# Kernel tuning notes

Hardware: AMD Instinct MI355X
Metric: run time of the kernel (lower is better)

## Reference

```python
import jax, jax.numpy as jnp
import numpy as np

N_NODES = 100000
N_EDGES = 600000
IN_FEAT = 128
OUT_FEAT = 128
NUM_RELS = 8
NUM_BASES = 4


def setup_inputs() -> dict:
    key = jax.random.key(0)
    ks = jax.random.split(key, 8)
    h = jax.random.normal(ks[0], (N_NODES, IN_FEAT), dtype=jnp.float32)
    # xavier-ish scale for params
    weight = jax.random.normal(ks[1], (NUM_BASES, IN_FEAT, OUT_FEAT), dtype=jnp.float32) * (1.0 / np.sqrt(IN_FEAT))
    w_comp = jax.random.normal(ks[2], (NUM_RELS, NUM_BASES), dtype=jnp.float32) * (1.0 / np.sqrt(NUM_BASES))
    root_weight = jax.random.normal(ks[3], (IN_FEAT, OUT_FEAT), dtype=jnp.float32) * (1.0 / np.sqrt(IN_FEAT))
    bias = jnp.zeros((OUT_FEAT,), dtype=jnp.float32)
    src = jax.random.randint(ks[4], (N_EDGES,), 0, N_NODES, dtype=jnp.int32)
    dst = jax.random.randint(ks[5], (N_EDGES,), 0, N_NODES, dtype=jnp.int32)
    rel_type = jax.random.randint(ks[6], (N_EDGES,), 0, NUM_RELS, dtype=jnp.int32)
    return {"h": h, "weight": weight, "w_comp": w_comp, "root_weight": root_weight,
            "bias": bias, "src": src, "dst": dst, "rel_type": rel_type}


def reference(h, weight, w_comp, root_weight, bias, src, dst, rel_type):
    # Basis decomposition: W[r] = sum_b w_comp[r,b] * weight[b]
    B, I, O = weight.shape
    R = w_comp.shape[0]
    W = (w_comp @ weight.reshape(B, I * O)).reshape(R, I, O)  # [R, in, out]
    # msg_e = h[src_e] @ W[rel_e]; computed as all-relation projection + gather
    # (avoids materializing [E, in, out] per-edge weights)
    proj = jnp.einsum('ni,rio->nro', h, W)          # [N, R, out]
    msg = proj[src, rel_type]                        # [E, out]
    agg = jax.ops.segment_sum(msg, dst, num_segments=h.shape[0])  # scatter-sum
    out = h @ root_weight + agg + bias
    return jax.nn.relu(out)
```

## Files before the change

### kernel.cpp

```cpp
#include <hip/hip_runtime.h>
#include <hip/hip_bf16.h>

#define N_NODES 100000
#define N_EDGES 600000
#define FEAT 128
#define NUM_RELS 8
#define NUM_BASES 4
#define NBE 2344

#define PREP_CAST 6250
#define PREP_BLDB 320
#define PREP_ZERO 392
#define PREP_GRID (PREP_CAST + PREP_BLDB + PREP_ZERO)

#define SCAN_TILES 98

typedef short bf16x8 __attribute__((ext_vector_type(8)));
typedef float f32x4  __attribute__((ext_vector_type(4)));
typedef float f32x2  __attribute__((ext_vector_type(2)));

__device__ inline short f2bf(float x) {
    __hip_bfloat16 b = __float2bfloat16(x);
    return *reinterpret_cast<short*>(&b);
}


__global__ __launch_bounds__(256) void k_prep(const float* __restrict__ h,
                                              const float* __restrict__ weight,
                                              const float* __restrict__ rw,
                                              short* __restrict__ hb,
                                              short* __restrict__ Bt,
                                              int* __restrict__ cnt,
                                              int* __restrict__ status) {
    int b = blockIdx.x;
    if (b < PREP_CAST) {
        int i = b * 256 + threadIdx.x;
        const float4* h4 = (const float4*)h;
        float4 v0 = h4[2 * i], v1 = h4[2 * i + 1];
        union { short s[8]; bf16x8 v; } u;
        u.s[0] = f2bf(v0.x); u.s[1] = f2bf(v0.y); u.s[2] = f2bf(v0.z); u.s[3] = f2bf(v0.w);
        u.s[4] = f2bf(v1.x); u.s[5] = f2bf(v1.y); u.s[6] = f2bf(v1.z); u.s[7] = f2bf(v1.w);
        ((bf16x8*)hb)[i] = u.v;
    } else if (b < PREP_CAST + PREP_BLDB) {
        int idx = (b - PREP_CAST) * 256 + threadIdx.x;
        int kc = idx >> 14;
        int e  = idx & 16383;
        int o  = e >> 7, ip = e & 127;
        float v = (kc == 0) ? rw[ip * FEAT + o]
                            : weight[(kc - 1) * FEAT * FEAT + ip * FEAT + o];
        Bt[idx] = f2bf(v);
    } else {
        int i = (b - PREP_CAST - PREP_BLDB) * 256 + threadIdx.x;
        if (i < N_NODES) cnt[i] = 0;
        else if (i - N_NODES < 128) status[i - N_NODES] = 0;
    }
}

__global__ __launch_bounds__(256) void k_hist_dst(const int* __restrict__ dst,
                                                  int* __restrict__ cnt) {
    int i = blockIdx.x * 256 + threadIdx.x;
    if (i < N_EDGES) atomicAdd(&cnt[dst[i]], 1);
}

__global__ __launch_bounds__(256) void k_scan_lb(const int* __restrict__ cnt,
                                                 int* __restrict__ offs,
                                                 int* __restrict__ cursor,
                                                 int* __restrict__ status) {
    __shared__ int wsum[4];
    __shared__ int bcast;
    int bid = blockIdx.x;
    int lane = threadIdx.x & 63, wid = threadIdx.x >> 6;
    const int N4 = N_NODES / 4;
    int i4 = bid * 256 + threadIdx.x;

    const int4* cnt4 = (const int4*)cnt;
    int4 v = (i4 < N4) ? cnt4[i4] : make_int4(0, 0, 0, 0);
    int s = v.x + v.y + v.z + v.w;
    int incl = s;
#pragma unroll
    for (int d = 1; d < 64; d <<= 1) {
        int t = __shfl_up(incl, d);
        if (lane >= d) incl += t;
    }
    if (lane == 63) wsum[wid] = incl;
    __syncthreads();
    if (threadIdx.x == 0) {
        int a = 0;
#pragma unroll
        for (int w = 0; w < 4; ++w) { int x = wsum[w]; wsum[w] = a; a += x; }
        int total = a;
        __hip_atomic_store(&status[bid], (total << 2) | 1,
                           __ATOMIC_RELEASE, __HIP_MEMORY_SCOPE_AGENT);
        int excl = 0;
        for (int t = bid - 1; t >= 0; ) {
            int st = __hip_atomic_load(&status[t],
                                       __ATOMIC_ACQUIRE, __HIP_MEMORY_SCOPE_AGENT);
            if ((st & 3) == 0) { __builtin_amdgcn_s_sleep(1); continue; }
            excl += st >> 2;
            if ((st & 3) == 2) break;
            --t;
        }
        __hip_atomic_store(&status[bid], ((excl + total) << 2) | 2,
                           __ATOMIC_RELEASE, __HIP_MEMORY_SCOPE_AGENT);
        bcast = excl;
        if (bid == SCAN_TILES - 1) offs[N_NODES] = excl + total;
    }
    __syncthreads();
    int base = bcast + wsum[wid] + incl - s;
    if (i4 < N4) {
        int4 ex;
        ex.x = base;
        ex.y = base + v.x;
        ex.z = base + v.x + v.y;
        ex.w = base + v.x + v.y + v.z;
        ((int4*)offs)[i4]   = ex;
        ((int4*)cursor)[i4] = ex;
    }
}

__global__ __launch_bounds__(256) void k_scatter_sorted(const int* __restrict__ src,
                                                        const int* __restrict__ dst,
                                                        const int* __restrict__ rel,
                                                        int* __restrict__ cursor,
                                                        int* __restrict__ packed) {
    int e = blockIdx.x * 256 + threadIdx.x;
    if (e < N_EDGES) {
        int p = atomicAdd(&cursor[dst[e]], 1);
        packed[p] = (src[e] << 3) | rel[e];
    }
}

__global__ __launch_bounds__(256) void k_edge_z(const int* __restrict__ offs,
                                                const int* __restrict__ packed,
                                                const float* __restrict__ wc,
                                                const short* __restrict__ hb,
                                                unsigned int* __restrict__ z_u32) {
    int wid = threadIdx.x >> 6, lane = threadIdx.x & 63;
    int d = blockIdx.x * 4 + wid;
    if (d >= N_NODES) return;
    int s = offs[d], e = offs[d + 1];

    const float4* wc4 = (const float4*)wc;
    const unsigned int* hbu = (const unsigned int*)hb;

    f32x2 z2[4] = {(f32x2)0.f, (f32x2)0.f, (f32x2)0.f, (f32x2)0.f};

    for (int base = s; base < e; base += 64) {
        int rem = e - base;
        int m = rem < 64 ? rem : 64;
        int pk = (lane < m) ? packed[base + lane] : 0;
        int j = 0;
        for (; j + 3 < m; j += 4) {
            int p0 = __builtin_amdgcn_readlane(pk, j);
            int p1 = __builtin_amdgcn_readlane(pk, j + 1);
            int p2 = __builtin_amdgcn_readlane(pk, j + 2);
            int p3 = __builtin_amdgcn_readlane(pk, j + 3);
            unsigned int v0 = hbu[(size_t)(p0 >> 3) * 64 + lane];
            unsigned int v1 = hbu[(size_t)(p1 >> 3) * 64 + lane];
            unsigned int v2 = hbu[(size_t)(p2 >> 3) * 64 + lane];
            unsigned int v3 = hbu[(size_t)(p3 >> 3) * 64 + lane];
            float4 c0 = wc4[p0 & 7];
            float4 c1 = wc4[p1 & 7];
            float4 c2 = wc4[p2 & 7];
            float4 c3 = wc4[p3 & 7];
            f32x2 h0; h0.x = __int_as_float(v0 << 16); h0.y = __int_as_float(v0 & 0xffff0000u);
            f32x2 h1; h1.x = __int_as_float(v1 << 16); h1.y = __int_as_float(v1 & 0xffff0000u);
            f32x2 h2; h2.x = __int_as_float(v2 << 16); h2.y = __int_as_float(v2 & 0xffff0000u);
            f32x2 h3; h3.x = __int_as_float(v3 << 16); h3.y = __int_as_float(v3 & 0xffff0000u);
            f32x2 cc;
            cc = c0.x; z2[0] += cc * h0;
            cc = c0.y; z2[1] += cc * h0;
            cc = c0.z; z2[2] += cc * h0;
            cc = c0.w; z2[3] += cc * h0;
            cc = c1.x; z2[0] += cc * h1;
            cc = c1.y; z2[1] += cc * h1;
            cc = c1.z; z2[2] += cc * h1;
            cc = c1.w; z2[3] += cc * h1;
            cc = c2.x; z2[0] += cc * h2;
            cc = c2.y; z2[1] += cc * h2;
            cc = c2.z; z2[2] += cc * h2;
            cc = c2.w; z2[3] += cc * h2;
            cc = c3.x; z2[0] += cc * h3;
            cc = c3.y; z2[1] += cc * h3;
            cc = c3.z; z2[2] += cc * h3;
            cc = c3.w; z2[3] += cc * h3;
        }
        for (; j < m; ++j) {
            int p0 = __builtin_amdgcn_readlane(pk, j);
            unsigned int v0 = hbu[(size_t)(p0 >> 3) * 64 + lane];
            float4 c0 = wc4[p0 & 7];
            f32x2 h0; h0.x = __int_as_float(v0 << 16); h0.y = __int_as_float(v0 & 0xffff0000u);
            f32x2 cc;
            cc = c0.x; z2[0] += cc * h0;
            cc = c0.y; z2[1] += cc * h0;
            cc = c0.z; z2[2] += cc * h0;
            cc = c0.w; z2[3] += cc * h0;
        }
    }

    unsigned int* row = z_u32 + (size_t)d * 256;
#pragma unroll
    for (int b = 0; b < 4; ++b) {
        unsigned int lo = ((unsigned int)(unsigned short)f2bf(z2[b].x));
        unsigned int hi = ((unsigned int)(unsigned short)f2bf(z2[b].y)) << 16;
        row[b * 64 + lane] = lo | hi;
    }
}

__global__ __launch_bounds__(256) void k_gemm_fused(const short* __restrict__ hb,
                                                    const short* __restrict__ z,
                                                    const short* __restrict__ Bt,
                                                    const float* __restrict__ bias,
                                                    float* __restrict__ out) {
    __shared__ short lds[FEAT * FEAT];
    int wave = threadIdx.x >> 6, lane = threadIdx.x & 63;
    int quad = lane >> 4, n16 = lane & 15;
    int base = blockIdx.x * 128 + wave * 32;

    int rowA0 = base + n16;        if (rowA0 >= N_NODES) rowA0 = N_NODES - 1;
    int rowA1 = base + 16 + n16;   if (rowA1 >= N_NODES) rowA1 = N_NODES - 1;

    f32x4 acc[2][8];
#pragma unroll
    for (int mt = 0; mt < 2; ++mt)
#pragma unroll
        for (int nt = 0; nt < 8; ++nt) acc[mt][nt] = (f32x4)0.f;

    float4* l4 = (float4*)lds;
    const bf16x8* bp = (const bf16x8*)lds;

    for (int kc = 0; kc < 5; ++kc) {
        if (kc) __syncthreads();
        const float4* s4 = (const float4*)(Bt + kc * FEAT * FEAT);
#pragma unroll
        for (int t = 0; t < 8; ++t) {
            int linear = threadIdx.x + t * 256;
            int o = linear >> 4, c = linear & 15;
            l4[(o << 4) + ((c + (o >> 3)) & 15)] = s4[linear];
        }
        __syncthreads();

        const bf16x8* a0p = (kc == 0)
            ? (const bf16x8*)(hb + (size_t)rowA0 * FEAT)
            : (const bf16x8*)(z + (size_t)rowA0 * 512 + (kc - 1) * FEAT);
        const bf16x8* a1p = (kc == 0)
            ? (const bf16x8*)(hb + (size_t)rowA1 * FEAT)
            : (const bf16x8*)(z + (size_t)rowA1 * 512 + (kc - 1) * FEAT);

#pragma unroll
        for (int ks = 0; ks < 4; ++ks) {
            bf16x8 a0 = a0p[ks * 4 + quad];
            bf16x8 a1 = a1p[ks * 4 + quad];
            int sw = (ks * 4 + quad + n16) & 15;
#pragma unroll
            for (int nt = 0; nt < 8; ++nt) {
                int o = n16 * 8 + nt;
                bf16x8 b = bp[(o << 4) + sw];
                acc[0][nt] = __builtin_amdgcn_mfma_f32_16x16x32_bf16(a0, b, acc[0][nt], 0, 0, 0);
                acc[1][nt] = __builtin_amdgcn_mfma_f32_16x16x32_bf16(a1, b, acc[1][nt], 0, 0, 0);
            }
        }
    }

    float bv[8];
#pragma unroll
    for (int nt = 0; nt < 8; ++nt) bv[nt] = bias[n16 * 8 + nt];

#pragma unroll
    for (int mt = 0; mt < 2; ++mt)
#pragma unroll
        for (int reg = 0; reg < 4; ++reg) {
            int node = base + mt * 16 + quad * 4 + reg;
            if (node < N_NODES) {
                float4 fa, fb;
                fa.x = fmaxf(acc[mt][0][reg] + bv[0], 0.f);
                fa.y = fmaxf(acc[mt][1][reg] + bv[1], 0.f);
                fa.z = fmaxf(acc[mt][2][reg] + bv[2], 0.f);
                fa.w = fmaxf(acc[mt][3][reg] + bv[3], 0.f);
                fb.x = fmaxf(acc[mt][4][reg] + bv[4], 0.f);
                fb.y = fmaxf(acc[mt][5][reg] + bv[5], 0.f);
                fb.z = fmaxf(acc[mt][6][reg] + bv[6], 0.f);
                fb.w = fmaxf(acc[mt][7][reg] + bv[7], 0.f);
                float* row = out + (size_t)node * FEAT + n16 * 8;
                *(float4*)row       = fa;
                *(float4*)(row + 4) = fb;
            }
        }
}


extern "C" void kernel_launch(void* const* d_in, const int* in_sizes, int n_in,
                              void* d_out, int out_size, void* d_ws, size_t ws_size,
                              hipStream_t stream) {
    const float* h    = (const float*)d_in[0];
    const float* wgt  = (const float*)d_in[1];
    const float* wcmp = (const float*)d_in[2];
    const float* rw   = (const float*)d_in[3];
    const float* bias = (const float*)d_in[4];
    const int*   src  = (const int*)d_in[5];
    const int*   dst  = (const int*)d_in[6];
    const int*   rel  = (const int*)d_in[7];
    float* out = (float*)d_out;

    char* ws = (char*)d_ws;
    short*        hb     = (short*)(ws + 0);
    short*        Bt     = (short*)(ws + 25600000ull);
    short*        z      = (short*)(ws + 25763840ull);
    unsigned int* z_u32  = (unsigned int*)z;
    int*          packed = (int*)(ws + 128163840ull);
    int*          cnt    = (int*)(ws + 130563840ull);
    int*          offs   = (int*)(ws + 130963840ull);
    int*          cursor = (int*)(ws + 131363968ull);
    int*          status = (int*)(ws + 131763968ull);

    hipLaunchKernelGGL(k_prep,     dim3(PREP_GRID), dim3(256), 0, stream,
                       h, wgt, rw, hb, Bt, cnt, status);
    hipLaunchKernelGGL(k_hist_dst, dim3(NBE),  dim3(256), 0, stream, dst, cnt);
    hipLaunchKernelGGL(k_scan_lb,  dim3(SCAN_TILES), dim3(256), 0, stream,
                       cnt, offs, cursor, status);
    hipLaunchKernelGGL(k_scatter_sorted, dim3(NBE), dim3(256), 0, stream,
                       src, dst, rel, cursor, packed);
    hipLaunchKernelGGL(k_edge_z,   dim3((N_NODES + 3) / 4), dim3(256), 0, stream,
                       offs, packed, wcmp, hb, z_u32);
    hipLaunchKernelGGL(k_gemm_fused, dim3((N_NODES + 127) / 128), dim3(256), 0, stream,
                       hb, z, Bt, bias, out);
}
```

Baseline: 270.7 us.

## Pre-swizzle B in global memory and stage it with direct global-to-LDS loads

The prep kernel now writes the bf16 weight matrix already in the swizzled LDS layout. The GEMM then copies it with global_load_lds DMA instead of a register round trip. Each block's tile drops from 128 to 64 rows, so the grid doubles and each wave uses fewer accumulator registers, which may raise occupancy. The cost is that every block now reloads all five 32KB B chunks for half as many rows, roughly doubling B traffic and barrier count per unit of work.

```diff
diff --git a/kernel.cpp b/kernel.cpp
--- a/kernel.cpp
+++ b/kernel.cpp
@@ -48,7 +48,9 @@
         int o  = e >> 7, ip = e & 127;
         float v = (kc == 0) ? rw[ip * FEAT + o]
                             : weight[(kc - 1) * FEAT * FEAT + ip * FEAT + o];
-        Bt[idx] = f2bf(v);
+        int c = ip >> 3, r = ip & 7;
+        int L = (o << 4) | ((c + (o >> 3)) & 15);
+        Bt[kc * 16384 + L * 8 + r] = f2bf(v);
     } else {
         int i = (b - PREP_CAST - PREP_BLDB) * 256 + threadIdx.x;
         if (i < N_NODES) cnt[i] = 0;
@@ -215,49 +217,44 @@
     __shared__ short lds[FEAT * FEAT];
     int wave = threadIdx.x >> 6, lane = threadIdx.x & 63;
     int quad = lane >> 4, n16 = lane & 15;
-    int base = blockIdx.x * 128 + wave * 32;
-
-    int rowA0 = base + n16;        if (rowA0 >= N_NODES) rowA0 = N_NODES - 1;
-    int rowA1 = base + 16 + n16;   if (rowA1 >= N_NODES) rowA1 = N_NODES - 1;
-
-    f32x4 acc[2][8];
-#pragma unroll
-    for (int mt = 0; mt < 2; ++mt)
-#pragma unroll
-        for (int nt = 0; nt < 8; ++nt) acc[mt][nt] = (f32x4)0.f;
-
-    float4* l4 = (float4*)lds;
+    int base = blockIdx.x * 64 + wave * 16;
+
+    int rowA = base + n16;
+    if (rowA >= N_NODES) rowA = N_NODES - 1;
+
+    f32x4 acc[8];
+#pragma unroll
+    for (int nt = 0; nt < 8; ++nt) acc[nt] = (f32x4)0.f;
+
     const bf16x8* bp = (const bf16x8*)lds;
+    char* lds_base = (char*)lds;
 
     for (int kc = 0; kc < 5; ++kc) {
         if (kc) __syncthreads();
-        const float4* s4 = (const float4*)(Bt + kc * FEAT * FEAT);
+        const char* gsrc = (const char*)Bt + kc * 32768;
 #pragma unroll
         for (int t = 0; t < 8; ++t) {
-            int linear = threadIdx.x + t * 256;
-            int o = linear >> 4, c = linear & 15;
-            l4[(o << 4) + ((c + (o >> 3)) & 15)] = s4[linear];
+            unsigned int off = wave * 8192 + t * 1024;
+            __builtin_amdgcn_global_load_lds(
+                (const __attribute__((address_space(1))) unsigned int*)(gsrc + off + lane * 16),
+                (__attribute__((address_space(3))) unsigned int*)(lds_base + off),
+                16, 0, 0);
         }
         __syncthreads();
 
-        const bf16x8* a0p = (kc == 0)
-            ? (const bf16x8*)(hb + (size_t)rowA0 * FEAT)
-            : (const bf16x8*)(z + (size_t)rowA0 * 512 + (kc - 1) * FEAT);
-        const bf16x8* a1p = (kc == 0)
-            ? (const bf16x8*)(hb + (size_t)rowA1 * FEAT)
-            : (const bf16x8*)(z + (size_t)rowA1 * 512 + (kc - 1) * FEAT);
+        const bf16x8* ap = (kc == 0)
+            ? (const bf16x8*)(hb + (size_t)rowA * FEAT)
+            : (const bf16x8*)(z + (size_t)rowA * 512 + (kc - 1) * FEAT);
 
 #pragma unroll
         for (int ks = 0; ks < 4; ++ks) {
-            bf16x8 a0 = a0p[ks * 4 + quad];
-            bf16x8 a1 = a1p[ks * 4 + quad];
+            bf16x8 a = ap[ks * 4 + quad];
             int sw = (ks * 4 + quad + n16) & 15;
 #pragma unroll
             for (int nt = 0; nt < 8; ++nt) {
                 int o = n16 * 8 + nt;
                 bf16x8 b = bp[(o << 4) + sw];
-                acc[0][nt] = __builtin_amdgcn_mfma_f32_16x16x32_bf16(a0, b, acc[0][nt], 0, 0, 0);
-                acc[1][nt] = __builtin_amdgcn_mfma_f32_16x16x32_bf16(a1, b, acc[1][nt], 0, 0, 0);
+                acc[nt] = __builtin_amdgcn_mfma_f32_16x16x32_bf16(a, b, acc[nt], 0, 0, 0);
             }
         }
     }
@@ -267,25 +264,23 @@
     for (int nt = 0; nt < 8; ++nt) bv[nt] = bias[n16 * 8 + nt];
 
 #pragma unroll
-    for (int mt = 0; mt < 2; ++mt)
-#pragma unroll
-        for (int reg = 0; reg < 4; ++reg) {
-            int node = base + mt * 16 + quad * 4 + reg;
-            if (node < N_NODES) {
-                float4 fa, fb;
-                fa.x = fmaxf(acc[mt][0][reg] + bv[0], 0.f);
-                fa.y = fmaxf(acc[mt][1][reg] + bv[1], 0.f);
-                fa.z = fmaxf(acc[mt][2][reg] + bv[2], 0.f);
-                fa.w = fmaxf(acc[mt][3][reg] + bv[3], 0.f);
-                fb.x = fmaxf(acc[mt][4][reg] + bv[4], 0.f);
-                fb.y = fmaxf(acc[mt][5][reg] + bv[5], 0.f);
-                fb.z = fmaxf(acc[mt][6][reg] + bv[6], 0.f);
-                fb.w = fmaxf(acc[mt][7][reg] + bv[7], 0.f);
-                float* row = out + (size_t)node * FEAT + n16 * 8;
-                *(float4*)row       = fa;
-                *(float4*)(row + 4) = fb;
-            }
-        }
+    for (int reg = 0; reg < 4; ++reg) {
+        int node = base + quad * 4 + reg;
+        if (node < N_NODES) {
+            float4 fa, fb;
+            fa.x = fmaxf(acc[0][reg] + bv[0], 0.f);
+            fa.y = fmaxf(acc[1][reg] + bv[1], 0.f);
+            fa.z = fmaxf(acc[2][reg] + bv[2], 0.f);
+            fa.w = fmaxf(acc[3][reg] + bv[3], 0.f);
+            fb.x = fmaxf(acc[4][reg] + bv[4], 0.f);
+            fb.y = fmaxf(acc[5][reg] + bv[5], 0.f);
+            fb.z = fmaxf(acc[6][reg] + bv[6], 0.f);
+            fb.w = fmaxf(acc[7][reg] + bv[7], 0.f);
+            float* row = out + (size_t)node * FEAT + n16 * 8;
+            *(float4*)row       = fa;
+            *(float4*)(row + 4) = fb;
+        }
+    }
 }
 
 
@@ -322,6 +317,6 @@
                        src, dst, rel, cursor, packed);
     hipLaunchKernelGGL(k_edge_z,   dim3((N_NODES + 3) / 4), dim3(256), 0, stream,
                        offs, packed, wcmp, hb, z_u32);
-    hipLaunchKernelGGL(k_gemm_fused, dim3((N_NODES + 127) / 128), dim3(256), 0, stream,
+    hipLaunchKernelGGL(k_gemm_fused, dim3((N_NODES + 63) / 64), dim3(256), 0, stream,
                        hb, z, Bt, bias, out);
 }
```

Result: no change. 265.8 us (-1.8%).

## Pre-swizzle weights into MFMA fragment layout and read B directly from global

Applied to the files above, without the earlier changes.

The prep kernel now writes the bf16 weight matrices already laid out per MFMA fragment (per k-step, n-tile and lane). This lets the fused GEMM load B operands straight from global/L2 instead of staging them through LDS with barriers. The GEMM becomes one wave per block handling 32 rows, and the bounds checks are dropped because N_NODES divides by 32. Each wave now reads the full 160KB of B from cache instead of sharing it through LDS, which raises L2 traffic, but it removes the LDS fills and barriers.

```diff
diff --git a/kernel.cpp b/kernel.cpp
--- a/kernel.cpp
+++ b/kernel.cpp
@@ -29,7 +29,7 @@
                                               const float* __restrict__ weight,
                                               const float* __restrict__ rw,
                                               short* __restrict__ hb,
-                                              short* __restrict__ Bt,
+                                              short* __restrict__ Btf,
                                               int* __restrict__ cnt,
                                               int* __restrict__ status) {
     int b = blockIdx.x;
@@ -48,7 +48,10 @@
         int o  = e >> 7, ip = e & 127;
         float v = (kc == 0) ? rw[ip * FEAT + o]
                             : weight[(kc - 1) * FEAT * FEAT + ip * FEAT + o];
-        Bt[idx] = f2bf(v);
+        int nt = o & 7, n16 = o >> 3;
+        int ks = ip >> 5, quad = (ip >> 3) & 3, j = ip & 7;
+        int lane = quad * 16 + n16;
+        Btf[((kc * 4 + ks) * 8 + nt) * 512 + lane * 8 + j] = f2bf(v);
     } else {
         int i = (b - PREP_CAST - PREP_BLDB) * 256 + threadIdx.x;
         if (i < N_NODES) cnt[i] = 0;
@@ -207,18 +210,17 @@
     }
 }
 
-__global__ __launch_bounds__(256) void k_gemm_fused(const short* __restrict__ hb,
-                                                    const short* __restrict__ z,
-                                                    const short* __restrict__ Bt,
-                                                    const float* __restrict__ bias,
-                                                    float* __restrict__ out) {
-    __shared__ short lds[FEAT * FEAT];
-    int wave = threadIdx.x >> 6, lane = threadIdx.x & 63;
+__global__ __launch_bounds__(64) void k_gemm_fused(const short* __restrict__ hb,
+                                                   const short* __restrict__ z,
+                                                   const short* __restrict__ Btf,
+                                                   const float* __restrict__ bias,
+                                                   float* __restrict__ out) {
+    int lane = threadIdx.x;
     int quad = lane >> 4, n16 = lane & 15;
-    int base = blockIdx.x * 128 + wave * 32;
-
-    int rowA0 = base + n16;        if (rowA0 >= N_NODES) rowA0 = N_NODES - 1;
-    int rowA1 = base + 16 + n16;   if (rowA1 >= N_NODES) rowA1 = N_NODES - 1;
+    int base = blockIdx.x * 32;
+
+    int rowA0 = base + n16;
+    int rowA1 = base + 16 + n16;
 
     f32x4 acc[2][8];
 #pragma unroll
@@ -226,20 +228,9 @@
 #pragma unroll
         for (int nt = 0; nt < 8; ++nt) acc[mt][nt] = (f32x4)0.f;
 
-    float4* l4 = (float4*)lds;
-    const bf16x8* bp = (const bf16x8*)lds;
+    const bf16x8* bf = (const bf16x8*)Btf;
 
     for (int kc = 0; kc < 5; ++kc) {
-        if (kc) __syncthreads();
-        const float4* s4 = (const float4*)(Bt + kc * FEAT * FEAT);
-#pragma unroll
-        for (int t = 0; t < 8; ++t) {
-            int linear = threadIdx.x + t * 256;
-            int o = linear >> 4, c = linear & 15;
-            l4[(o << 4) + ((c + (o >> 3)) & 15)] = s4[linear];
-        }
-        __syncthreads();
-
         const bf16x8* a0p = (kc == 0)
             ? (const bf16x8*)(hb + (size_t)rowA0 * FEAT)
             : (const bf16x8*)(z + (size_t)rowA0 * 512 + (kc - 1) * FEAT);
@@ -251,11 +242,10 @@
         for (int ks = 0; ks < 4; ++ks) {
             bf16x8 a0 = a0p[ks * 4 + quad];
             bf16x8 a1 = a1p[ks * 4 + quad];
-            int sw = (ks * 4 + quad + n16) & 15;
+            const bf16x8* bks = bf + ((kc * 4 + ks) * 8) * 64 + lane;
 #pragma unroll
             for (int nt = 0; nt < 8; ++nt) {
-                int o = n16 * 8 + nt;
-                bf16x8 b = bp[(o << 4) + sw];
+                bf16x8 b = bks[nt * 64];
                 acc[0][nt] = __builtin_amdgcn_mfma_f32_16x16x32_bf16(a0, b, acc[0][nt], 0, 0, 0);
                 acc[1][nt] = __builtin_amdgcn_mfma_f32_16x16x32_bf16(a1, b, acc[1][nt], 0, 0, 0);
             }
@@ -271,20 +261,18 @@
 #pragma unroll
         for (int reg = 0; reg < 4; ++reg) {
             int node = base + mt * 16 + quad * 4 + reg;
-            if (node < N_NODES) {
-                float4 fa, fb;
-                fa.x = fmaxf(acc[mt][0][reg] + bv[0], 0.f);
-                fa.y = fmaxf(acc[mt][1][reg] + bv[1], 0.f);
-                fa.z = fmaxf(acc[mt][2][reg] + bv[2], 0.f);
-                fa.w = fmaxf(acc[mt][3][reg] + bv[3], 0.f);
-                fb.x = fmaxf(acc[mt][4][reg] + bv[4], 0.f);
-                fb.y = fmaxf(acc[mt][5][reg] + bv[5], 0.f);
-                fb.z = fmaxf(acc[mt][6][reg] + bv[6], 0.f);
-                fb.w = fmaxf(acc[mt][7][reg] + bv[7], 0.f);
-                float* row = out + (size_t)node * FEAT + n16 * 8;
-                *(float4*)row       = fa;
-                *(float4*)(row + 4) = fb;
-            }
+            float4 fa, fb;
+            fa.x = fmaxf(acc[mt][0][reg] + bv[0], 0.f);
+            fa.y = fmaxf(acc[mt][1][reg] + bv[1], 0.f);
+            fa.z = fmaxf(acc[mt][2][reg] + bv[2], 0.f);
+            fa.w = fmaxf(acc[mt][3][reg] + bv[3], 0.f);
+            fb.x = fmaxf(acc[mt][4][reg] + bv[4], 0.f);
+            fb.y = fmaxf(acc[mt][5][reg] + bv[5], 0.f);
+            fb.z = fmaxf(acc[mt][6][reg] + bv[6], 0.f);
+            fb.w = fmaxf(acc[mt][7][reg] + bv[7], 0.f);
+            float* row = out + (size_t)node * FEAT + n16 * 8;
+            *(float4*)row       = fa;
+            *(float4*)(row + 4) = fb;
         }
 }
 
@@ -304,7 +292,7 @@
 
     char* ws = (char*)d_ws;
     short*        hb     = (short*)(ws + 0);
-    short*        Bt     = (short*)(ws + 25600000ull);
+    short*        Btf    = (short*)(ws + 25600000ull);
     short*        z      = (short*)(ws + 25763840ull);
     unsigned int* z_u32  = (unsigned int*)z;
     int*          packed = (int*)(ws + 128163840ull);
@@ -314,7 +302,7 @@
     int*          status = (int*)(ws + 131763968ull);
 
     hipLaunchKernelGGL(k_prep,     dim3(PREP_GRID), dim3(256), 0, stream,
-                       h, wgt, rw, hb, Bt, cnt, status);
+                       h, wgt, rw, hb, Btf, cnt, status);
     hipLaunchKernelGGL(k_hist_dst, dim3(NBE),  dim3(256), 0, stream, dst, cnt);
     hipLaunchKernelGGL(k_scan_lb,  dim3(SCAN_TILES), dim3(256), 0, stream,
                        cnt, offs, cursor, status);
@@ -322,6 +310,6 @@
                        src, dst, rel, cursor, packed);
     hipLaunchKernelGGL(k_edge_z,   dim3((N_NODES + 3) / 4), dim3(256), 0, stream,
                        offs, packed, wcmp, hb, z_u32);
-    hipLaunchKernelGGL(k_gemm_fused, dim3((N_NODES + 127) / 128), dim3(256), 0, stream,
-                       hb, z, Bt, bias, out);
-}
+    hipLaunchKernelGGL(k_gemm_fused, dim3(N_NODES / 32), dim3(64), 0, stream,
+                       hb, z, Btf, bias, out);
+}
```

New measurement: 294.0 us. 1.09x slower.
